# Performance work log

Hardware: AMD Instinct MI355X
Metric: run time of the kernel (lower is better)

Reference implementation:

```python
import jax, jax.numpy as jnp
import numpy as np

# Hardcoded capability requirements per task (3 capabilities x 13 tasks), as in the source.
CAP_MATRIX = 0.01 * np.array([
    [0.0, 33.0, 50.0, 43.0, 56.0, 67.0, 62.0, 47.0, 50.0, 51.0, 64.0, 64.0, 68.0],
    [0.0, 33.0, 49.0, 39.0, 58.0, 67.0, 60.0, 54.0, 52.0, 52.0, 67.0, 69.0, 71.0],
    [0.0, 33.0, 42.0, 39.0, 44.0, 52.0, 49.0, 42.0, 45.0, 46.0, 52.0, 53.0, 56.0],
], dtype=np.float32)  # [3, 13]

T_TASKS = 64      # tasks per observation sequence
B_SEQS = 262144   # number of observation sequences
N_TASK_IDS = 13
CAP_DIM = 3


def setup_inputs() -> dict:
    key = jax.random.key(0)
    k1, k2, k3, k4, k5 = jax.random.split(key, 5)
    # Performance encoding must avoid the invalid (1,1) combo:
    # state 0 -> (0,0) no info; state 1 -> (0,1) success; state 2 -> (1,0) failure.
    state = jax.random.randint(k1, (T_TASKS, B_SEQS), 0, 3)
    inptasksperf = jnp.stack(
        [(state == 2).astype(jnp.int32), (state == 1).astype(jnp.int32)], axis=-1
    )  # [T, B, 2]
    tasksobsids = jax.random.randint(k2, (T_TASKS, B_SEQS, 1), 0, N_TASK_IDS).astype(jnp.int32)
    taskspredids = jax.random.randint(k3, (B_SEQS, 1), 0, N_TASK_IDS).astype(jnp.int32)
    inptasksobs = jnp.zeros((T_TASKS, B_SEQS, 1), jnp.float32)  # only shapes are used
    betas = 20.0 * jax.random.uniform(k4, (CAP_DIM,), jnp.float32)
    zetas = jax.random.uniform(k5, (CAP_DIM,), jnp.float32)
    return {
        "inptasksobs": inptasksobs,
        "inptasksperf": inptasksperf,
        "tasksobsids": tasksobsids,
        "taskspredids": taskspredids,
        "num_obs_tasks": T_TASKS,
        "betas": betas,
        "zetas": zetas,
    }


def reference(inptasksobs, inptasksperf, tasksobsids, taskspredids, num_obs_tasks, betas, zetas):
    cap_table = jnp.asarray(CAP_MATRIX.T)                # [13, 3] per-task capability rows
    obs_cap = cap_table[tasksobsids[..., 0]]             # [T, B, 3]
    p0 = inptasksperf[..., 0] != 0                       # [T, B]
    p1 = inptasksperf[..., 1] != 0
    success = jnp.logical_and(~p0, p1)                   # (0,1) -> success
    failure = jnp.logical_and(p0, ~p1)                   # (1,0) -> failure; (0,0) -> skip

    def step(cap, x):
        oc, s, f = x                                     # oc [B,3], s/f [B]
        cap = jnp.where(s[:, None], jnp.maximum(cap, oc), cap)
        cap = jnp.where(f[:, None], jnp.minimum(cap, oc), cap)
        return cap, None

    cap0 = jnp.zeros((obs_cap.shape[1], CAP_DIM), jnp.float32)
    cap, _ = jax.lax.scan(step, cap0, (obs_cap, success, failure))  # [B, 3]

    req = cap_table[taskspredids[:, 0]]                  # [B, 3]
    p = betas * (req - cap)                              # [B, 3]
    trust = jnp.prod((1.0 + jnp.exp(p)) ** (-zetas), axis=-1, keepdims=True)  # [B, 1]
    return trust
```

## Files before the change

kernel.cpp:

```cpp
#include <hip/hip_runtime.h>

#define T_TASKS 64
#define B_SEQS 262144
#define BLOCK 256
#define HALF_T 32
#define DEPTH 8

#define POS_BIG  3.402823466e+38f
#define NEG_BIG -3.402823466e+38f

__constant__ float c_capT[13][4] = {
    {0.00f, 0.00f, 0.00f, 0.f}, {0.33f, 0.33f, 0.33f, 0.f},
    {0.50f, 0.49f, 0.42f, 0.f}, {0.43f, 0.39f, 0.39f, 0.f},
    {0.56f, 0.58f, 0.44f, 0.f}, {0.67f, 0.67f, 0.52f, 0.f},
    {0.62f, 0.60f, 0.49f, 0.f}, {0.47f, 0.54f, 0.42f, 0.f},
    {0.50f, 0.52f, 0.45f, 0.f}, {0.51f, 0.52f, 0.46f, 0.f},
    {0.64f, 0.67f, 0.52f, 0.f}, {0.64f, 0.69f, 0.53f, 0.f},
    {0.68f, 0.71f, 0.56f, 0.f},
};

#define STEP(l, h, A, B)                          \
    l = __builtin_amdgcn_fmed3f(l, A, B);         \
    h = __builtin_amdgcn_fmed3f(h, A, B);

__global__ __launch_bounds__(BLOCK) void trust_kernel(
    const int4* __restrict__ perf2,
    const int2* __restrict__ obs2,
    const int2* __restrict__ pred2,
    const float* __restrict__ betas,
    const float* __restrict__ zetas,
    float2* __restrict__ out2)
{
    __shared__ float4 s_cap[13];
    __shared__ float  s_lh[2][128][13];

    if (threadIdx.x < 13)
        s_cap[threadIdx.x] = *(const float4*)&c_capT[threadIdx.x][0];
    __syncthreads();

    const int tid = threadIdx.x;
    const int c   = tid >> 7;
    const int pr  = tid & 127;
    const size_t pair      = (size_t)blockIdx.x * 128 + pr;
    const size_t rowStride = B_SEQS / 2;
    const size_t base      = (size_t)(c * HALF_T) * rowStride + pair;

    int4 pfa[DEPTH];
    int2 ida[DEPTH];
    #pragma unroll
    for (int i = 0; i < DEPTH; ++i) {
        pfa[i] = perf2[base + (size_t)i * rowStride];
        ida[i] = obs2 [base + (size_t)i * rowStride];
    }

    float la0=NEG_BIG, la1=NEG_BIG, la2=NEG_BIG;
    float ha0=POS_BIG, ha1=POS_BIG, ha2=POS_BIG;
    float lb0=NEG_BIG, lb1=NEG_BIG, lb2=NEG_BIG;
    float hb0=POS_BIG, hb1=POS_BIG, hb2=POS_BIG;

    #pragma unroll
    for (int t = 0; t < HALF_T; ++t) {
        const int  slot = t & (DEPTH - 1);
        const int4 pf = pfa[slot];
        const int2 id = ida[slot];
        if (t + DEPTH < HALF_T) {
            pfa[slot] = perf2[base + (size_t)(t + DEPTH) * rowStride];
            ida[slot] = obs2 [base + (size_t)(t + DEPTH) * rowStride];
        }
        const float4 oa = s_cap[id.x];
        const float4 ob = s_cap[id.y];
        const bool sa = (pf.x == 0) && (pf.y != 0);
        const bool fa = (pf.x != 0) && (pf.y == 0);
        const bool sb = (pf.z == 0) && (pf.w != 0);
        const bool fb = (pf.z != 0) && (pf.w == 0);

        const float Aa0 = sa ? oa.x : NEG_BIG, Ba0 = fa ? oa.x : POS_BIG;
        const float Aa1 = sa ? oa.y : NEG_BIG, Ba1 = fa ? oa.y : POS_BIG;
        const float Aa2 = sa ? oa.z : NEG_BIG, Ba2 = fa ? oa.z : POS_BIG;
        const float Ab0 = sb ? ob.x : NEG_BIG, Bb0 = fb ? ob.x : POS_BIG;
        const float Ab1 = sb ? ob.y : NEG_BIG, Bb1 = fb ? ob.y : POS_BIG;
        const float Ab2 = sb ? ob.z : NEG_BIG, Bb2 = fb ? ob.z : POS_BIG;

        STEP(la0, ha0, Aa0, Ba0)
        STEP(la1, ha1, Aa1, Ba1)
        STEP(la2, ha2, Aa2, Ba2)
        STEP(lb0, hb0, Ab0, Bb0)
        STEP(lb1, hb1, Ab1, Bb1)
        STEP(lb2, hb2, Ab2, Bb2)
    }

    float* dst = &s_lh[c][pr][0];
    dst[0]=la0; dst[1]=la1; dst[2]=la2; dst[3]=ha0; dst[4]=ha1; dst[5]=ha2;
    dst[6]=lb0; dst[7]=lb1; dst[8]=lb2; dst[9]=hb0; dst[10]=hb1; dst[11]=hb2;
    __syncthreads();

    if (tid < 128) {
        const float* q0 = &s_lh[0][tid][0];
        const float* q1 = &s_lh[1][tid][0];

        float ca0 = fminf(fmaxf(0.0f, q0[0]), q0[3]);
        float ca1 = fminf(fmaxf(0.0f, q0[1]), q0[4]);
        float ca2 = fminf(fmaxf(0.0f, q0[2]), q0[5]);
        ca0 = fminf(fmaxf(ca0, q1[0]), q1[3]);
        ca1 = fminf(fmaxf(ca1, q1[1]), q1[4]);
        ca2 = fminf(fmaxf(ca2, q1[2]), q1[5]);

        float cb0 = fminf(fmaxf(0.0f, q0[6]), q0[9]);
        float cb1 = fminf(fmaxf(0.0f, q0[7]), q0[10]);
        float cb2 = fminf(fmaxf(0.0f, q0[8]), q0[11]);
        cb0 = fminf(fmaxf(cb0, q1[6]), q1[9]);
        cb1 = fminf(fmaxf(cb1, q1[7]), q1[10]);
        cb2 = fminf(fmaxf(cb2, q1[8]), q1[11]);

        const size_t pair = (size_t)blockIdx.x * 128 + tid;
        const int2 pid = pred2[pair];
        const float4 ra = s_cap[pid.x];
        const float4 rb = s_cap[pid.y];
        const float be0 = betas[0], be1 = betas[1], be2 = betas[2];
        const float ze0 = zetas[0], ze1 = zetas[1], ze2 = zetas[2];

        const float ta = powf(1.0f + expf(be0 * (ra.x - ca0)), -ze0)
                       * powf(1.0f + expf(be1 * (ra.y - ca1)), -ze1)
                       * powf(1.0f + expf(be2 * (ra.z - ca2)), -ze2);
        const float tb = powf(1.0f + expf(be0 * (rb.x - cb0)), -ze0)
                       * powf(1.0f + expf(be1 * (rb.y - cb1)), -ze1)
                       * powf(1.0f + expf(be2 * (rb.z - cb2)), -ze2);

        out2[pair] = make_float2(ta, tb);
    }
}

extern "C" void kernel_launch(void* const* d_in, const int* in_sizes, int n_in,
                              void* d_out, int out_size, void* d_ws, size_t ws_size,
                              hipStream_t stream) {
    const int4*  perf2 = (const int4*)d_in[1];
    const int2*  obs2  = (const int2*)d_in[2];
    const int2*  pred2 = (const int2*)d_in[3];
    const float* betas = (const float*)d_in[5];
    const float* zetas = (const float*)d_in[6];
    float2* out2 = (float2*)d_out;

    const int blocks = B_SEQS / 256;
    trust_kernel<<<blocks, BLOCK, 0, stream>>>(perf2, obs2, pred2, betas, zetas, out2);
}
```

Measured before the change: 268.0 us.

## Split time scan into eight chunks per sequence pair with all loads issued upfront

Each block now handles 32 sequence pairs, and 8 threads per pair each scan an 8-step chunk of the time dimension instead of 2 threads each scanning 32 steps. All loads for a chunk are issued before any compute, replacing the rolling prefetch ring. A shared-memory median combine merges the chunks, and the epilogue runs one sequence per thread. The aim is more memory-level parallelism and a shorter serial dependency chain. The cost is 4x more blocks, a larger combine step and narrower 32-lane coalesced segments per row.

New measurement: 269.5 us. About the same (+0.5%).

```diff
diff --git a/kernel.cpp b/kernel.cpp
--- a/kernel.cpp
+++ b/kernel.cpp
@@ -3,8 +3,9 @@
 #define T_TASKS 64
 #define B_SEQS 262144
 #define BLOCK 256
-#define HALF_T 32
-#define DEPTH 8
+#define CHUNKS 8
+#define TPC 8
+#define PAIRS 32
 
 #define POS_BIG  3.402823466e+38f
 #define NEG_BIG -3.402823466e+38f
@@ -23,35 +24,37 @@
     l = __builtin_amdgcn_fmed3f(l, A, B);         \
     h = __builtin_amdgcn_fmed3f(h, A, B);
 
-__global__ __launch_bounds__(BLOCK) void trust_kernel(
+__global__ __launch_bounds__(BLOCK, 4) void trust_kernel(
     const int4* __restrict__ perf2,
     const int2* __restrict__ obs2,
-    const int2* __restrict__ pred2,
+    const int*  __restrict__ predids,
     const float* __restrict__ betas,
     const float* __restrict__ zetas,
-    float2* __restrict__ out2)
+    float* __restrict__ out)
 {
     __shared__ float4 s_cap[13];
-    __shared__ float  s_lh[2][128][13];
+    __shared__ float  s_lh[CHUNKS][2 * PAIRS][7];
 
     if (threadIdx.x < 13)
         s_cap[threadIdx.x] = *(const float4*)&c_capT[threadIdx.x][0];
     __syncthreads();
 
     const int tid = threadIdx.x;
-    const int c   = tid >> 7;
-    const int pr  = tid & 127;
-    const size_t pair      = (size_t)blockIdx.x * 128 + pr;
+    const int ps  = tid & (PAIRS - 1);
+    const int c   = tid >> 5;
     const size_t rowStride = B_SEQS / 2;
-    const size_t base      = (size_t)(c * HALF_T) * rowStride + pair;
+    const size_t pair = (size_t)blockIdx.x * PAIRS + ps;
+    const size_t base = (size_t)(c * TPC) * rowStride + pair;
 
-    int4 pfa[DEPTH];
-    int2 ida[DEPTH];
+    int4 pf[TPC];
+    int2 idv[TPC];
     #pragma unroll
-    for (int i = 0; i < DEPTH; ++i) {
-        pfa[i] = perf2[base + (size_t)i * rowStride];
-        ida[i] = obs2 [base + (size_t)i * rowStride];
-    }
+    for (int i = 0; i < TPC; ++i)
+        pf[i] = perf2[base + (size_t)i * rowStride];
+    #pragma unroll
+    for (int i = 0; i < TPC; ++i)
+        idv[i] = obs2[base + (size_t)i * rowStride];
+    __builtin_amdgcn_sched_barrier(0);
 
     float la0=NEG_BIG, la1=NEG_BIG, la2=NEG_BIG;
     float ha0=POS_BIG, ha1=POS_BIG, ha2=POS_BIG;
@@ -59,20 +62,13 @@
     float hb0=POS_BIG, hb1=POS_BIG, hb2=POS_BIG;
 
     #pragma unroll
-    for (int t = 0; t < HALF_T; ++t) {
-        const int  slot = t & (DEPTH - 1);
-        const int4 pf = pfa[slot];
-        const int2 id = ida[slot];
-        if (t + DEPTH < HALF_T) {
-            pfa[slot] = perf2[base + (size_t)(t + DEPTH) * rowStride];
-            ida[slot] = obs2 [base + (size_t)(t + DEPTH) * rowStride];
-        }
-        const float4 oa = s_cap[id.x];
-        const float4 ob = s_cap[id.y];
-        const bool sa = (pf.x == 0) && (pf.y != 0);
-        const bool fa = (pf.x != 0) && (pf.y == 0);
-        const bool sb = (pf.z == 0) && (pf.w != 0);
-        const bool fb = (pf.z != 0) && (pf.w == 0);
+    for (int i = 0; i < TPC; ++i) {
+        const float4 oa = s_cap[idv[i].x];
+        const float4 ob = s_cap[idv[i].y];
+        const bool sa = (pf[i].x == 0) && (pf[i].y != 0);
+        const bool fa = (pf[i].x != 0) && (pf[i].y == 0);
+        const bool sb = (pf[i].z == 0) && (pf[i].w != 0);
+        const bool fb = (pf[i].z != 0) && (pf[i].w == 0);
 
         const float Aa0 = sa ? oa.x : NEG_BIG, Ba0 = fa ? oa.x : POS_BIG;
         const float Aa1 = sa ? oa.y : NEG_BIG, Ba1 = fa ? oa.y : POS_BIG;
@@ -89,57 +85,47 @@
         STEP(lb2, hb2, Ab2, Bb2)
     }
 
-    float* dst = &s_lh[c][pr][0];
-    dst[0]=la0; dst[1]=la1; dst[2]=la2; dst[3]=ha0; dst[4]=ha1; dst[5]=ha2;
-    dst[6]=lb0; dst[7]=lb1; dst[8]=lb2; dst[9]=hb0; dst[10]=hb1; dst[11]=hb2;
+    float* da = &s_lh[c][2 * ps][0];
+    da[0]=la0; da[1]=la1; da[2]=la2; da[3]=ha0; da[4]=ha1; da[5]=ha2;
+    float* db = &s_lh[c][2 * ps + 1][0];
+    db[0]=lb0; db[1]=lb1; db[2]=lb2; db[3]=hb0; db[4]=hb1; db[5]=hb2;
     __syncthreads();
 
-    if (tid < 128) {
-        const float* q0 = &s_lh[0][tid][0];
-        const float* q1 = &s_lh[1][tid][0];
+    if (tid < 2 * PAIRS) {
+        float x0 = 0.0f, x1 = 0.0f, x2 = 0.0f;
+        #pragma unroll
+        for (int cc = 0; cc < CHUNKS; ++cc) {
+            const float* q = &s_lh[cc][tid][0];
+            x0 = fminf(fmaxf(x0, q[0]), q[3]);
+            x1 = fminf(fmaxf(x1, q[1]), q[4]);
+            x2 = fminf(fmaxf(x2, q[2]), q[5]);
+        }
+        const size_t seq = (size_t)blockIdx.x * (2 * PAIRS) + tid;
+        const int pid = predids[seq];
+        const float4 r = s_cap[pid];
 
-        float ca0 = fminf(fmaxf(0.0f, q0[0]), q0[3]);
-        float ca1 = fminf(fmaxf(0.0f, q0[1]), q0[4]);
-        float ca2 = fminf(fmaxf(0.0f, q0[2]), q0[5]);
-        ca0 = fminf(fmaxf(ca0, q1[0]), q1[3]);
-        ca1 = fminf(fmaxf(ca1, q1[1]), q1[4]);
-        ca2 = fminf(fmaxf(ca2, q1[2]), q1[5]);
+        const float q0 = betas[0] * (r.x - x0);
+        const float q1 = betas[1] * (r.y - x1);
+        const float q2 = betas[2] * (r.z - x2);
 
-        float cb0 = fminf(fmaxf(0.0f, q0[6]), q0[9]);
-        float cb1 = fminf(fmaxf(0.0f, q0[7]), q0[10]);
-        float cb2 = fminf(fmaxf(0.0f, q0[8]), q0[11]);
-        cb0 = fminf(fmaxf(cb0, q1[6]), q1[9]);
-        cb1 = fminf(fmaxf(cb1, q1[7]), q1[10]);
-        cb2 = fminf(fmaxf(cb2, q1[8]), q1[11]);
+        const float t0 = powf(1.0f + expf(q0), -zetas[0]);
+        const float t1 = powf(1.0f + expf(q1), -zetas[1]);
+        const float t2 = powf(1.0f + expf(q2), -zetas[2]);
 
-        const size_t pair = (size_t)blockIdx.x * 128 + tid;
-        const int2 pid = pred2[pair];
-        const float4 ra = s_cap[pid.x];
-        const float4 rb = s_cap[pid.y];
-        const float be0 = betas[0], be1 = betas[1], be2 = betas[2];
-        const float ze0 = zetas[0], ze1 = zetas[1], ze2 = zetas[2];
-
-        const float ta = powf(1.0f + expf(be0 * (ra.x - ca0)), -ze0)
-                       * powf(1.0f + expf(be1 * (ra.y - ca1)), -ze1)
-                       * powf(1.0f + expf(be2 * (ra.z - ca2)), -ze2);
-        const float tb = powf(1.0f + expf(be0 * (rb.x - cb0)), -ze0)
-                       * powf(1.0f + expf(be1 * (rb.y - cb1)), -ze1)
-                       * powf(1.0f + expf(be2 * (rb.z - cb2)), -ze2);
-
-        out2[pair] = make_float2(ta, tb);
+        out[seq] = t0 * t1 * t2;
     }
 }
 
 extern "C" void kernel_launch(void* const* d_in, const int* in_sizes, int n_in,
                               void* d_out, int out_size, void* d_ws, size_t ws_size,
                               hipStream_t stream) {
-    const int4*  perf2 = (const int4*)d_in[1];
-    const int2*  obs2  = (const int2*)d_in[2];
-    const int2*  pred2 = (const int2*)d_in[3];
-    const float* betas = (const float*)d_in[5];
-    const float* zetas = (const float*)d_in[6];
-    float2* out2 = (float2*)d_out;
+    const int4*  perf2   = (const int4*)d_in[1];
+    const int2*  obs2    = (const int2*)d_in[2];
+    const int*   predids = (const int*)d_in[3];
+    const float* betas   = (const float*)d_in[5];
+    const float* zetas   = (const float*)d_in[6];
+    float* out = (float*)d_out;
 
-    const int blocks = B_SEQS / 256;
-    trust_kernel<<<blocks, BLOCK, 0, stream>>>(perf2, obs2, pred2, betas, zetas, out2);
+    const int blocks = B_SEQS / (2 * PAIRS);
+    trust_kernel<<<blocks, BLOCK, 0, stream>>>(perf2, obs2, predids, betas, zetas, out);
 }
```
